# Optimization experiments

Measured on AMD Instinct MI355X. Metric: run time of the kernel, lower is better.

Reference implementation:

```python
import jax, jax.numpy as jnp
import numpy as np

# Bit-slice widths from SliceMethod([1,2,4]) on both input and weight sides
# (MSB-first, 7 magnitude bits total, sign carried per-element in each slice).
IN_SLICES = (1, 2, 4)
W_SLICES = (1, 2, 4)


def _l2norm(a):
    # F.normalize(a, p=2, dim=1)
    n = jnp.sqrt(jnp.sum(a * a, axis=1, keepdims=True))
    return a / jnp.maximum(n, 1e-12)


def _quantize(a, nbits):
    # symmetric fixed-point quantization to `nbits` magnitude bits,
    # dynamic per-tensor scale (bw_e=None -> fixed-point path)
    Q = float(2 ** nbits - 1)
    scale = jnp.max(jnp.abs(a))
    q = jnp.round(a / scale * Q)  # integer-valued float32 in [-Q, Q]
    return q, scale / Q


def _bit_slices(q, widths):
    # split |q| into bit groups (MSB-first per slice_method order); sign is
    # folded into each slice so recombination sum_k 2^off_k * slice_k == q
    sign = jnp.sign(q)
    mag = jnp.abs(q)
    total = sum(widths)
    slices = []
    off = total
    for w in widths:
        off -= w
        s = jnp.mod(jnp.floor(mag / (2.0 ** off)), 2.0 ** w)
        slices.append((sign * s, off))
    return slices


def setup_inputs() -> dict:
    key = jax.random.key(0)
    kx, kw = jax.random.split(key)
    x = jax.random.normal(kx, (4096, 1024), dtype=jnp.float32)
    weight = jax.random.normal(kw, (8192, 1024), dtype=jnp.float32)  # vectors.t -> [M, D]
    return {"x": x, "weight": weight}


def reference(x, weight):
    xn = _l2norm(x)        # [B, D]
    wn = _l2norm(weight)   # [M, D]
    qx, sx = _quantize(xn, sum(IN_SLICES))
    qw, sw = _quantize(wn, sum(W_SLICES))
    x_slices = _bit_slices(qx, IN_SLICES)
    w_slices = _bit_slices(qw, W_SLICES)
    # map_reduce_dot_func: 9 slice-pair low-bit GEMMs, recombined with 2^(oi+oj)
    acc = jnp.zeros((x.shape[0], weight.shape[0]), dtype=jnp.float32)
    for xs_k, ox in x_slices:
        for ws_k, ow in w_slices:
            acc = acc + (2.0 ** (ox + ow)) * jnp.einsum('bd,md->bm', xs_k, ws_k)
    cos = acc * sx * sw  # dequantize -> cosine similarity in [-1, 1]
    return 1.0 - cos
```

## Files before the change

kernel.cpp:

```cpp
#include <hip/hip_runtime.h>
#include <cstdint>
#include <cstddef>


#define D_COLS 1024
#define M_ROWS 4096
#define N_ROWS 8192

using i32x4 = __attribute__((ext_vector_type(4))) int;

__device__ __forceinline__ void gload_lds16(const void* g, void* lds) {
  __builtin_amdgcn_global_load_lds(
      (const __attribute__((address_space(1))) uint32_t*)g,
      (__attribute__((address_space(3))) uint32_t*)lds, 16, 0, 0);
}

__global__ __launch_bounds__(256) void rownorm_kernel(
    const float* __restrict__ x, const float* __restrict__ w,
    float* __restrict__ invnorm, float* __restrict__ rmax) {
  const int row = blockIdx.x;
  const float* a = (row < M_ROWS) ? x + (size_t)row * D_COLS
                                  : w + (size_t)(row - M_ROWS) * D_COLS;
  const float4 v = ((const float4*)a)[threadIdx.x];
  float ss = v.x * v.x + v.y * v.y + v.z * v.z + v.w * v.w;
  float mx = fmaxf(fmaxf(fabsf(v.x), fabsf(v.y)), fmaxf(fabsf(v.z), fabsf(v.w)));
#pragma unroll
  for (int off = 32; off; off >>= 1) {
    ss += __shfl_down(ss, off, 64);
    mx = fmaxf(mx, __shfl_down(mx, off, 64));
  }
  __shared__ float s_ss[4], s_mx[4];
  const int wave = threadIdx.x >> 6, lane = threadIdx.x & 63;
  if (lane == 0) { s_ss[wave] = ss; s_mx[wave] = mx; }
  __syncthreads();
  if (threadIdx.x == 0) {
    float tss = (s_ss[0] + s_ss[1]) + (s_ss[2] + s_ss[3]);
    float tmx = fmaxf(fmaxf(s_mx[0], s_mx[1]), fmaxf(s_mx[2], s_mx[3]));
    float inv = 1.0f / fmaxf(sqrtf(tss), 1e-12f);
    invnorm[row] = inv;
    rmax[row] = tmx * inv;
  }
}

__global__ __launch_bounds__(1024) void scale_reduce_kernel(
    const float* __restrict__ rmax, float* __restrict__ scales) {
  const int t = threadIdx.x;
  float mx = 0.f, mw = 0.f;
  for (int i = t; i < M_ROWS; i += 1024) mx = fmaxf(mx, rmax[i]);
  for (int i = t; i < N_ROWS; i += 1024) mw = fmaxf(mw, rmax[M_ROWS + i]);
#pragma unroll
  for (int off = 32; off; off >>= 1) {
    mx = fmaxf(mx, __shfl_down(mx, off, 64));
    mw = fmaxf(mw, __shfl_down(mw, off, 64));
  }
  __shared__ float smx[16], smw[16];
  const int wave = t >> 6, lane = t & 63;
  if (lane == 0) { smx[wave] = mx; smw[wave] = mw; }
  __syncthreads();
  if (t == 0) {
    float a = 0.f, b = 0.f;
#pragma unroll
    for (int i = 0; i < 16; ++i) { a = fmaxf(a, smx[i]); b = fmaxf(b, smw[i]); }
    scales[0] = a;
    scales[1] = b;
  }
}

__global__ __launch_bounds__(256) void quant_fused_kernel(
    const float* __restrict__ x, const float* __restrict__ w,
    const float* __restrict__ invnorm, const float* __restrict__ scales,
    uint4* __restrict__ qx, uint4* __restrict__ qw) {
  __shared__ uint4 T[128][16];
  const int b = blockIdx.x;
  const float* a;
  const float* inv;
  float sc;
  uint4* img;
  int bb;
  if (b < 128) { a = x; inv = invnorm; sc = scales[0]; img = qx; bb = b; }
  else { a = w; inv = invnorm + M_ROWS; sc = scales[1]; img = qw; bb = b - 128; }
  const int t = threadIdx.x;
  const int g = bb & 3;
  const int Q = bb >> 2;
  const float s = 127.0f / sc;

  const int cc_l = t & 15;
  const int tr = t >> 4;
#pragma unroll
  for (int rc = 0; rc < 8; ++rc) {
    const int rl = rc * 16 + tr;
    const int r = Q * 128 + rl;
    const float f = inv[r] * s;
    const float4* src = (const float4*)(a + (size_t)r * D_COLS + (g * 16 + cc_l) * 16);
    unsigned pk[4];
#pragma unroll
    for (int q = 0; q < 4; ++q) {
      const float4 v = src[q];
      const int q0 = (int)rintf(v.x * f), q1 = (int)rintf(v.y * f);
      const int q2 = (int)rintf(v.z * f), q3 = (int)rintf(v.w * f);
      pk[q] = (unsigned)(q0 & 0xff) | ((unsigned)(q1 & 0xff) << 8) |
              ((unsigned)(q2 & 0xff) << 16) | ((unsigned)(q3 & 0xff) << 24);
    }
    T[rl][cc_l ^ (rl & 15)] = make_uint4(pk[0], pk[1], pk[2], pk[3]);
  }
  __syncthreads();

  const int cc_w = g * 16 + (t >> 4);
  const int rw = t & 15;
  uint4* dst = img + (size_t)(Q * 16 + (cc_w >> 2)) * 512 + (cc_w & 3) * 128;
#pragma unroll
  for (int i = 0; i < 8; ++i) {
    const int rl = i * 16 + rw;
    dst[rl] = T[rl][(t >> 4) ^ (rl & 15)];
  }
}

__global__ __launch_bounds__(512, 4) void gemm_i8_kernel(
    const char* __restrict__ qx, const char* __restrict__ qw,
    const float* __restrict__ sx, const float* __restrict__ sw,
    float* __restrict__ out) {
  __shared__ __align__(16) char L[49152];
  const int t = threadIdx.x;
  const int wave = t >> 6, lane = t & 63;
  const int wr = wave >> 1, wc = wave & 1;
  const int rl = lane & 15, ko = lane >> 4;

  const int fid = blockIdx.x;
  const int swz = (fid & 7) * 128 + (fid >> 3);
  const int bx = swz & 63;
  const int by = swz >> 6;

  const char* sa0 = qx + (size_t)(2 * by) * 16 * 8192;
  const char* sa1 = qx + (size_t)(2 * by + 1) * 16 * 8192;
  const char* sb0 = qw + (size_t)bx * 16 * 8192;

  i32x4 acc[4][4] = {};
  const int woff = wave * 1024 + lane * 16;

#define ISSUE_HT(ks)                                                          \
  {                                                                           \
    const size_t so_ = (size_t)(ks) * 8192;                                   \
    char* d_ = L + ((ks) & 1) * 24576 + wave * 1024;                          \
    gload_lds16(sa0 + so_ + woff, d_);                                        \
    gload_lds16(sa1 + so_ + woff, d_ + 8192);                                 \
    gload_lds16(sb0 + so_ + woff, d_ + 16384);                                \
  }

#define STEP(ks, VM)                                                          \
  {                                                                           \
    if ((ks) + 1 < 16) ISSUE_HT((ks) + 1);                                    \
    asm volatile("s_waitcnt vmcnt(" #VM ")" ::: "memory");                    \
    asm volatile("s_barrier" ::: "memory");                                   \
    const char* Ab_ = L + ((ks) & 1) * 24576 + (wr >> 1) * 8192;              \
    const char* Bb_ = L + ((ks) & 1) * 24576 + 16384;                         \
    i32x4 af_[4], bf_[4];                                                     \
    _Pragma("unroll") for (int m_ = 0; m_ < 4; ++m_)                          \
      af_[m_] = *(const i32x4*)(Ab_ +                                         \
          (ko * 128 + (wr & 1) * 64 + m_ * 16 + rl) * 16);                    \
    _Pragma("unroll") for (int n_ = 0; n_ < 4; ++n_)                          \
      bf_[n_] = *(const i32x4*)(Bb_ +                                         \
          (ko * 128 + wc * 64 + n_ * 16 + rl) * 16);                          \
    __builtin_amdgcn_s_setprio(1);                                            \
    _Pragma("unroll") for (int m_ = 0; m_ < 4; ++m_)                          \
      _Pragma("unroll") for (int n_ = 0; n_ < 4; ++n_)                        \
        acc[m_][n_] = __builtin_amdgcn_mfma_i32_16x16x64_i8(                  \
            af_[m_], bf_[n_], acc[m_][n_], 0, 0, 0);                          \
    __builtin_amdgcn_s_setprio(0);                                            \
    asm volatile("s_barrier" ::: "memory");                                   \
  }

  ISSUE_HT(0);

#pragma unroll 1
  for (int ks = 0; ks < 15; ++ks) STEP(ks, 3);
  STEP(15, 0);
#undef STEP
#undef ISSUE_HT

  const float cs = sx[0] * sw[0] * (1.0f / 16129.0f);
  const int rowBase = by * 256 + wr * 64;
  const int colBase = bx * 128 + wc * 64;
#pragma unroll
  for (int m = 0; m < 4; ++m) {
    const int row = rowBase + m * 16 + ko * 4;
#pragma unroll
    for (int n = 0; n < 4; ++n) {
      const int col = colBase + n * 16 + rl;
#pragma unroll
      for (int j = 0; j < 4; ++j)
        out[(size_t)(row + j) * N_ROWS + col] = 1.0f - (float)acc[m][n][j] * cs;
    }
  }
}

extern "C" void kernel_launch(void* const* d_in, const int* in_sizes, int n_in,
                              void* d_out, int out_size, void* d_ws, size_t ws_size,
                              hipStream_t stream) {
  const float* x = (const float*)d_in[0];
  const float* w = (const float*)d_in[1];
  float* out = (float*)d_out;

  char* ws = (char*)d_ws;
  char* qx = ws;
  char* qw = ws + (size_t)M_ROWS * D_COLS;
  float* invnorm = (float*)(ws + (size_t)(M_ROWS + N_ROWS) * D_COLS);
  float* rmax = invnorm + (M_ROWS + N_ROWS);
  float* scales = rmax + (M_ROWS + N_ROWS);

  rownorm_kernel<<<M_ROWS + N_ROWS, 256, 0, stream>>>(x, w, invnorm, rmax);
  scale_reduce_kernel<<<1, 1024, 0, stream>>>(rmax, scales);

  quant_fused_kernel<<<384, 256, 0, stream>>>(
      x, w, invnorm, scales, (uint4*)qx, (uint4*)qw);

  gemm_i8_kernel<<<dim3(1024), 512, 0, stream>>>(qx, qw, &scales[0], &scales[1], out);
}
```

Before: 76.60 us.

## Process two column tiles per block, overlapping first tile's epilogue with second's GEMM

Each block now computes two adjacent 256x128 output tiles, so the grid drops from 1024 to 512 blocks. The A (qx) tile is reloaded from global for each column tile rather than kept in LDS. The first tile's result stores are spread across the k-steps of the second tile, so output writes overlap MFMA work, and the prefetch for the second tile starts before the first finishes. This doubles accumulator registers (occupancy hint lowered to 2) and fully unrolls the k-loop, which risks lower occupancy and code bloat.

After: 76.36 us. About the same (-0.3%).

```diff
diff --git a/kernel.cpp b/kernel.cpp
--- a/kernel.cpp
+++ b/kernel.cpp
@@ -115,7 +115,7 @@
   }
 }
 
-__global__ __launch_bounds__(512, 4) void gemm_i8_kernel(
+__global__ __launch_bounds__(512, 2) void gemm_i8_kernel(
     const char* __restrict__ qx, const char* __restrict__ qw,
     const float* __restrict__ sx, const float* __restrict__ sw,
     float* __restrict__ out) {
@@ -126,33 +126,46 @@
   const int rl = lane & 15, ko = lane >> 4;
 
   const int fid = blockIdx.x;
-  const int swz = (fid & 7) * 128 + (fid >> 3);
-  const int bx = swz & 63;
-  const int by = swz >> 6;
+  const int loc = fid >> 3;
+  const int by = loc & 15;
+  const int bxh = (fid & 7) * 4 + (loc >> 4);
 
   const char* sa0 = qx + (size_t)(2 * by) * 16 * 8192;
   const char* sa1 = qx + (size_t)(2 * by + 1) * 16 * 8192;
-  const char* sb0 = qw + (size_t)bx * 16 * 8192;
-
-  i32x4 acc[4][4] = {};
+  const char* sb0 = qw + (size_t)(2 * bxh) * 16 * 8192;
+  const char* sb1 = qw + (size_t)(2 * bxh + 1) * 16 * 8192;
+  const int pcol0 = (2 * bxh) * 128;
+  const int pcol1 = (2 * bxh + 1) * 128;
+
+  const float cs = sx[0] * sw[0] * (1.0f / 16129.0f);
+
+  i32x4 accA[4][4] = {};
+  i32x4 accB[4][4] = {};
   const int woff = wave * 1024 + lane * 16;
 
-#define ISSUE_HT(ks)                                                          \
+#define ISSUE_HT(sbp, ks)                                                     \
   {                                                                           \
     const size_t so_ = (size_t)(ks) * 8192;                                   \
     char* d_ = L + ((ks) & 1) * 24576 + wave * 1024;                          \
     gload_lds16(sa0 + so_ + woff, d_);                                        \
     gload_lds16(sa1 + so_ + woff, d_ + 8192);                                 \
-    gload_lds16(sb0 + so_ + woff, d_ + 16384);                                \
-  }
-
-#define STEP(ks, VM)                                                          \
+    gload_lds16(sbp + so_ + woff, d_ + 16384);                                \
+  }
+
+#define STEP(HASG, SBN, KSN, CURB, DOST, MC, NC, PCOLB, ACC, PACC, VMN)       \
   {                                                                           \
-    if ((ks) + 1 < 16) ISSUE_HT((ks) + 1);                                    \
-    asm volatile("s_waitcnt vmcnt(" #VM ")" ::: "memory");                    \
+    if (HASG) ISSUE_HT(SBN, KSN);                                             \
+    if (DOST) {                                                               \
+      const int row0_ = by * 256 + wr * 64 + (MC) * 16 + ko * 4;              \
+      const int col_ = (PCOLB) + wc * 64 + (NC) * 16 + rl;                    \
+      _Pragma("unroll") for (int j_ = 0; j_ < 4; ++j_)                        \
+        out[(size_t)(row0_ + j_) * N_ROWS + col_] =                           \
+            1.0f - (float)PACC[MC][NC][j_] * cs;                              \
+    }                                                                         \
+    asm volatile("s_waitcnt vmcnt(" #VMN ")" ::: "memory");                   \
     asm volatile("s_barrier" ::: "memory");                                   \
-    const char* Ab_ = L + ((ks) & 1) * 24576 + (wr >> 1) * 8192;              \
-    const char* Bb_ = L + ((ks) & 1) * 24576 + 16384;                         \
+    const char* Ab_ = L + (CURB) * 24576 + (wr >> 1) * 8192;                  \
+    const char* Bb_ = L + (CURB) * 24576 + 16384;                             \
     i32x4 af_[4], bf_[4];                                                     \
     _Pragma("unroll") for (int m_ = 0; m_ < 4; ++m_)                          \
       af_[m_] = *(const i32x4*)(Ab_ +                                         \
@@ -163,32 +176,60 @@
     __builtin_amdgcn_s_setprio(1);                                            \
     _Pragma("unroll") for (int m_ = 0; m_ < 4; ++m_)                          \
       _Pragma("unroll") for (int n_ = 0; n_ < 4; ++n_)                        \
-        acc[m_][n_] = __builtin_amdgcn_mfma_i32_16x16x64_i8(                  \
-            af_[m_], bf_[n_], acc[m_][n_], 0, 0, 0);                          \
+        ACC[m_][n_] = __builtin_amdgcn_mfma_i32_16x16x64_i8(                  \
+            af_[m_], bf_[n_], ACC[m_][n_], 0, 0, 0);                          \
     __builtin_amdgcn_s_setprio(0);                                            \
     asm volatile("s_barrier" ::: "memory");                                   \
   }
 
-  ISSUE_HT(0);
-
-#pragma unroll 1
-  for (int ks = 0; ks < 15; ++ks) STEP(ks, 3);
-  STEP(15, 0);
+  ISSUE_HT(sb0, 0);
+
+  STEP(1, sb0, 1, 0, 0, 0, 0, 0, accA, accA, 3)
+  STEP(1, sb0, 2, 1, 0, 0, 0, 0, accA, accA, 3)
+  STEP(1, sb0, 3, 0, 0, 0, 0, 0, accA, accA, 3)
+  STEP(1, sb0, 4, 1, 0, 0, 0, 0, accA, accA, 3)
+  STEP(1, sb0, 5, 0, 0, 0, 0, 0, accA, accA, 3)
+  STEP(1, sb0, 6, 1, 0, 0, 0, 0, accA, accA, 3)
+  STEP(1, sb0, 7, 0, 0, 0, 0, 0, accA, accA, 3)
+  STEP(1, sb0, 8, 1, 0, 0, 0, 0, accA, accA, 3)
+  STEP(1, sb0, 9, 0, 0, 0, 0, 0, accA, accA, 3)
+  STEP(1, sb0, 10, 1, 0, 0, 0, 0, accA, accA, 3)
+  STEP(1, sb0, 11, 0, 0, 0, 0, 0, accA, accA, 3)
+  STEP(1, sb0, 12, 1, 0, 0, 0, 0, accA, accA, 3)
+  STEP(1, sb0, 13, 0, 0, 0, 0, 0, accA, accA, 3)
+  STEP(1, sb0, 14, 1, 0, 0, 0, 0, accA, accA, 3)
+  STEP(1, sb0, 15, 0, 0, 0, 0, 0, accA, accA, 3)
+  STEP(1, sb1, 0, 1, 0, 0, 0, 0, accA, accA, 3)
+
+  STEP(1, sb1, 1, 0, 1, 0, 0, pcol0, accB, accA, 7)
+  STEP(1, sb1, 2, 1, 1, 0, 1, pcol0, accB, accA, 7)
+  STEP(1, sb1, 3, 0, 1, 0, 2, pcol0, accB, accA, 7)
+  STEP(1, sb1, 4, 1, 1, 0, 3, pcol0, accB, accA, 7)
+  STEP(1, sb1, 5, 0, 1, 1, 0, pcol0, accB, accA, 7)
+  STEP(1, sb1, 6, 1, 1, 1, 1, pcol0, accB, accA, 7)
+  STEP(1, sb1, 7, 0, 1, 1, 2, pcol0, accB, accA, 7)
+  STEP(1, sb1, 8, 1, 1, 1, 3, pcol0, accB, accA, 7)
+  STEP(1, sb1, 9, 0, 1, 2, 0, pcol0, accB, accA, 7)
+  STEP(1, sb1, 10, 1, 1, 2, 1, pcol0, accB, accA, 7)
+  STEP(1, sb1, 11, 0, 1, 2, 2, pcol0, accB, accA, 7)
+  STEP(1, sb1, 12, 1, 1, 2, 3, pcol0, accB, accA, 7)
+  STEP(1, sb1, 13, 0, 1, 3, 0, pcol0, accB, accA, 7)
+  STEP(1, sb1, 14, 1, 1, 3, 1, pcol0, accB, accA, 7)
+  STEP(1, sb1, 15, 0, 1, 3, 2, pcol0, accB, accA, 7)
+  STEP(0, sb1, 0, 1, 1, 3, 3, pcol0, accB, accA, 4)
+
 #undef STEP
 #undef ISSUE_HT
 
-  const float cs = sx[0] * sw[0] * (1.0f / 16129.0f);
-  const int rowBase = by * 256 + wr * 64;
-  const int colBase = bx * 128 + wc * 64;
 #pragma unroll
   for (int m = 0; m < 4; ++m) {
-    const int row = rowBase + m * 16 + ko * 4;
+    const int row = by * 256 + wr * 64 + m * 16 + ko * 4;
 #pragma unroll
     for (int n = 0; n < 4; ++n) {
-      const int col = colBase + n * 16 + rl;
+      const int col = pcol1 + wc * 64 + n * 16 + rl;
 #pragma unroll
       for (int j = 0; j < 4; ++j)
-        out[(size_t)(row + j) * N_ROWS + col] = 1.0f - (float)acc[m][n][j] * cs;
+        out[(size_t)(row + j) * N_ROWS + col] = 1.0f - (float)accB[m][n][j] * cs;
     }
   }
 }
@@ -213,5 +254,5 @@
   quant_fused_kernel<<<384, 256, 0, stream>>>(
       x, w, invnorm, scales, (uint4*)qx, (uint4*)qw);
 
-  gemm_i8_kernel<<<dim3(1024), 512, 0, stream>>>(qx, qw, &scales[0], &scales[1], out);
-}
+  gemm_i8_kernel<<<dim3(512), 512, 0, stream>>>(qx, qw, &scales[0], &scales[1], out);
+}
```
